# Kernel optimization log

Measured on AMD Instinct MI355X. Metric: run time of the kernel, lower is better.

Reference implementation:

```python
import jax, jax.numpy as jnp
import numpy as np
from jax import lax

EPS = 1e-5

def _per_sample_conv(x, w, stride):
    # x: [B,C,H,W], w: [B,O,I,3,3] -> one conv per sample (hypernetwork weights)
    def one(xi, wi):
        return lax.conv_general_dilated(
            xi[None], wi, window_strides=(stride, stride),
            padding=((1, 1), (1, 1)),
            dimension_numbers=('NCHW', 'OIHW', 'NCHW'))[0]
    return jax.vmap(one)(x, w)

def _batchnorm_train(x, gamma, beta):
    # torch BatchNorm2d training mode: batch stats over (N,H,W), biased var
    mean = jnp.mean(x, axis=(0, 2, 3), keepdims=True)
    var = jnp.var(x, axis=(0, 2, 3), keepdims=True)
    xn = (x - mean) * lax.rsqrt(var + EPS)
    return xn * gamma[None, :, None, None] + beta[None, :, None, None]

def setup_inputs() -> dict:
    key = jax.random.key(0)
    k1, k2, k3 = jax.random.split(key, 3)
    B, C, H, W = 32, 64, 112, 112
    x = jax.random.normal(k1, (B, C, H, W), dtype=jnp.float32)
    conv1_w = jax.random.normal(k2, (B, C, C, 3, 3), dtype=jnp.float32)
    conv2_w = jax.random.normal(k3, (B, C, C, 3, 3), dtype=jnp.float32)
    gamma1 = jnp.ones((C,), jnp.float32)
    beta1 = jnp.zeros((C,), jnp.float32)
    gamma2 = jnp.ones((C,), jnp.float32)
    beta2 = jnp.zeros((C,), jnp.float32)
    return {"x": x, "conv1_w": conv1_w, "conv2_w": conv2_w,
            "gamma1": gamma1, "beta1": beta1, "gamma2": gamma2, "beta2": beta2}

def reference(x, conv1_w, conv2_w, gamma1, beta1, gamma2, beta2):
    residual = x  # downsample=False -> IdentityLayer
    out = _per_sample_conv(x, conv1_w, stride=1)
    out = jax.nn.relu(_batchnorm_train(out, gamma1, beta1))
    out = _per_sample_conv(out, conv2_w, stride=1)
    out = _batchnorm_train(out, gamma2, beta2)
    return jax.nn.relu(out + residual)
```

## Files before the change

kernel.cpp:

```cpp
#include <hip/hip_runtime.h>

#define HW   112
#define HW2  12544
#define CH   64
#define NB   32
#define PRW  113
#define NP   12655
#define POFF 128
#define PS   13056
#define NPC  (NB*HW2)
#define TPX  784

using u16 = unsigned short;
typedef __attribute__((ext_vector_type(8))) short bf16x8;
typedef __attribute__((ext_vector_type(4))) float f32x4;

__device__ __forceinline__ float b2f(u16 u) {
    union { unsigned int i; float f; } c;
    c.i = ((unsigned int)u) << 16;
    return c.f;
}
__device__ __forceinline__ u16 f2b(float f) {
    union { float f; unsigned int i; } c;
    c.f = f;
    unsigned int x = c.i;
    x += 0x7fffu + ((x >> 16) & 1u);
    return (u16)(x >> 16);
}

template<int MODE>
__global__ __launch_bounds__(448, 2)
void conv_mfma(const u16* __restrict__ img, const u16* __restrict__ wt,
               u16* __restrict__ outp, float* __restrict__ sums,
               const float* __restrict__ psums, const float* __restrict__ gamma,
               const float* __restrict__ beta)
{
    __shared__ u16 wl[36864];
    __shared__ u16 bt[32768];
    const int bid = (int)blockIdx.x;
    const int sid = (bid & 7) * 64 + (bid >> 3);
    const int b = sid >> 4, tile = sid & 15;
    const int p0 = tile * TPX;
    const int w0 = tile * 791 - 114;
    const int tid = threadIdx.x;
    const int lane = tid & 63, wave = tid >> 6;
    const int px = lane & 15, kg = lane >> 4;

    const u16* wtb = wt + (size_t)b * 36864;
    for (int c = tid; c < 4608; c += 448)
        *(bf16x8*)(wl + c * 8) = *(const bf16x8*)(wtb + c * 8);

    float sc0[8], bi0[8], sc1[8], bi1[8];
    if (MODE == 1) {
        const int q = tid & 3;
#pragma unroll
        for (int e = 0; e < 8; ++e) {
            int c0 = q * 8 + e, c1 = 32 + q * 8 + e;
            float m0 = psums[c0] * (1.f / NPC), m1 = psums[c1] * (1.f / NPC);
            float v0 = psums[64 + c0] * (1.f / NPC) - m0 * m0;
            float v1 = psums[64 + c1] * (1.f / NPC) - m1 * m1;
            sc0[e] = gamma[c0] * rsqrtf(v0 + 1e-5f); bi0[e] = beta[c0] - m0 * sc0[e];
            sc1[e] = gamma[c1] * rsqrtf(v1 + 1e-5f); bi1[e] = beta[c1] - m1 * sc1[e];
        }
    }

    {
        const u16* bp = img + ((size_t)(b * 2 + 0) * PS + POFF + w0) * 32;
        for (int c = tid; c < 4096; c += 448) {
            bf16x8 v = *(const bf16x8*)(bp + c * 8);
            if (MODE == 1) {
                int pt = w0 + (c >> 2);
                bool val = ((unsigned)pt < (unsigned)NP) && (pt % PRW != PRW - 1);
#pragma unroll
                for (int e = 0; e < 8; ++e) {
                    float t = b2f((u16)v[e]) * sc0[e] + bi0[e];
                    t = (val && t > 0.f) ? t : 0.f;
                    v[e] = (short)f2b(t);
                }
            }
            *(bf16x8*)(bt + c * 8) = v;
        }
    }
    __syncthreads();

    int lsf[7];
#pragma unroll
    for (int f = 0; f < 7; ++f) {
        const int pix = p0 + (wave * 7 + f) * 16 + px;
        lsf[f] = pix + pix / HW - w0;
    }

    f32x4 acc[7][4];
#pragma unroll
    for (int f = 0; f < 7; ++f)
#pragma unroll
        for (int m = 0; m < 4; ++m) acc[f][m] = (f32x4)0.f;

#pragma unroll
    for (int h = 0; h < 2; ++h) {
        if (h == 1) {
            __syncthreads();
            const u16* bp = img + ((size_t)(b * 2 + 1) * PS + POFF + w0) * 32;
            for (int c = tid; c < 4096; c += 448) {
                bf16x8 v = *(const bf16x8*)(bp + c * 8);
                if (MODE == 1) {
                    int pt = w0 + (c >> 2);
                    bool val = ((unsigned)pt < (unsigned)NP) && (pt % PRW != PRW - 1);
#pragma unroll
                    for (int e = 0; e < 8; ++e) {
                        float t = b2f((u16)v[e]) * sc1[e] + bi1[e];
                        t = (val && t > 0.f) ? t : 0.f;
                        v[e] = (short)f2b(t);
                    }
                }
                *(bf16x8*)(bt + c * 8) = v;
            }
            __syncthreads();
        }
#pragma unroll
        for (int tap = 0; tap < 9; ++tap) {
            const int off = (tap / 3 - 1) * PRW + (tap % 3 - 1);
            bf16x8 Af[4];
#pragma unroll
            for (int m = 0; m < 4; ++m)
                Af[m] = *(const bf16x8*)(wl + h * 18432 + tap * 2048 + kg * 512 + (m * 16 + px) * 8);
#pragma unroll
            for (int f = 0; f < 7; ++f) {
                bf16x8 Bf = *(const bf16x8*)(bt + (lsf[f] + off) * 32 + kg * 8);
#pragma unroll
                for (int m = 0; m < 4; ++m)
                    acc[f][m] = __builtin_amdgcn_mfma_f32_16x16x32_bf16(Af[m], Bf, acc[f][m], 0, 0, 0);
            }
        }
    }

    float s_[4][4], sq[4][4];
#pragma unroll
    for (int m = 0; m < 4; ++m)
#pragma unroll
        for (int q = 0; q < 4; ++q) { s_[m][q] = 0.f; sq[m][q] = 0.f; }

#pragma unroll
    for (int f = 0; f < 7; ++f) {
        const int pix  = p0 + (wave * 7 + f) * 16 + px;
        const int slot = pix + pix / HW;
#pragma unroll
        for (int m = 0; m < 4; ++m) {
            float v0 = acc[f][m][0], v1 = acc[f][m][1], v2 = acc[f][m][2], v3 = acc[f][m][3];
            s_[m][0] += v0; s_[m][1] += v1; s_[m][2] += v2; s_[m][3] += v3;
            sq[m][0] += v0 * v0; sq[m][1] += v1 * v1;
            sq[m][2] += v2 * v2; sq[m][3] += v3 * v3;
            uint2 pk;
            pk.x = ((unsigned)f2b(v1) << 16) | f2b(v0);
            pk.y = ((unsigned)f2b(v3) << 16) | f2b(v2);
            if (MODE == 0) {
                u16* dst = outp + ((size_t)(b * 2 + (m >> 1)) * PS + POFF + slot) * 32
                                + (m & 1) * 16 + kg * 4;
                *(uint2*)dst = pk;
            } else {
                u16* dst = outp + ((size_t)b * HW2 + pix) * 64 + m * 16 + kg * 4;
                *(uint2*)dst = pk;
            }
        }
    }
#pragma unroll
    for (int off = 1; off < 16; off <<= 1) {
#pragma unroll
        for (int m = 0; m < 4; ++m)
#pragma unroll
            for (int q = 0; q < 4; ++q) {
                s_[m][q] += __shfl_xor(s_[m][q], off);
                sq[m][q] += __shfl_xor(sq[m][q], off);
            }
    }
    __syncthreads();
    float* red = (float*)bt;
    if (px == 0) {
#pragma unroll
        for (int m = 0; m < 4; ++m)
#pragma unroll
            for (int q = 0; q < 4; ++q) {
                int c = m * 16 + kg * 4 + q;
                red[wave * 128 + c]      = s_[m][q];
                red[wave * 128 + 64 + c] = sq[m][q];
            }
    }
    __syncthreads();
    if (tid < 128) {
        float t = 0.f;
#pragma unroll
        for (int k = 0; k < 7; ++k) t += red[k * 128 + tid];
        atomicAdd(&sums[tid], t);
    }
}

__global__ __launch_bounds__(256)
void xpad_kernel(const float* __restrict__ x, u16* __restrict__ img)
{
    const int b  = blockIdx.y;
    const int y  = blockIdx.x * 2 + (threadIdx.x >> 7);
    const int px = threadIdx.x & 127;
    if (px >= HW) return;
    const float* xr = x + (size_t)b * CH * HW2 + (size_t)y * HW + px;
#pragma unroll
    for (int cg = 0; cg < 8; ++cg) {
        bf16x8 pk;
#pragma unroll
        for (int j = 0; j < 8; ++j)
            pk[j] = (short)f2b(xr[(size_t)(cg * 8 + j) * HW2]);
        u16* op = img + ((size_t)(b * 2 + (cg >> 2)) * PS + POFF + (size_t)y * PRW + px) * 32
                      + (cg & 3) * 8;
        *(bf16x8*)op = pk;
    }
}

__global__ void border_kernel(u16* __restrict__ a, u16* __restrict__ y1,
                              float* __restrict__ st)
{
    if (blockIdx.x == 256) {
        if (threadIdx.x < 256) st[threadIdx.x] = 0.f;
        return;
    }
    int t = blockIdx.x * 256 + threadIdx.x;
    u16* buf = (t >= 32768) ? y1 : a;
    int t2 = t & 32767;
    int bh = t2 >> 9;
    int s  = t2 & 511;
    int slot;
    if (s < POFF)            slot = s;
    else if (s < POFF + 273) slot = POFF + NP + (s - POFF);
    else                     slot = POFF + (s - (POFF + 273)) * PRW + (PRW - 1);
    float4* q = (float4*)(buf + ((size_t)bh * PS + slot) * 32);
#pragma unroll
    for (int i = 0; i < 4; ++i) q[i] = (float4){0.f, 0.f, 0.f, 0.f};
}

__global__ __launch_bounds__(256)
void repack2_kernel(const float* __restrict__ w1, const float* __restrict__ w2,
                    u16* __restrict__ wt1, u16* __restrict__ wt2)
{
    int i = blockIdx.x * 256 + threadIdx.x;
    const int N = NB * 36864;
    const float* w = (i < N) ? w1 : w2;
    u16* wt = (i < N) ? wt1 : wt2;
    int o = (i < N) ? i : i - N;
    int b = o / 36864, r = o - b * 36864;
    int half = r / 18432; r -= half * 18432;
    int tap  = r / 2048;  r -= tap * 2048;
    int kq   = r / 512;   r -= kq * 512;
    int co   = r / 8;
    int ci   = half * 32 + kq * 8 + (r & 7);
    wt[o] = f2b(w[(((size_t)b * 64 + co) * 64 + ci) * 9 + tap]);
}

__global__ __launch_bounds__(256)
void finalize_kernel(const u16* __restrict__ y2, const float* __restrict__ sums,
                     const float* __restrict__ gamma, const float* __restrict__ beta,
                     const float* __restrict__ x, float* __restrict__ out)
{
    __shared__ float lt[64][116];
    __shared__ float sbl[128];
    const int b = blockIdx.y, y = blockIdx.x;
    const int tid = threadIdx.x;
    if (tid < 64) {
        float mean = sums[tid] * (1.f / NPC);
        float var  = sums[64 + tid] * (1.f / NPC) - mean * mean;
        float sc   = gamma[tid] * rsqrtf(var + 1e-5f);
        sbl[tid]      = sc;
        sbl[64 + tid] = beta[tid] - mean * sc;
    }
    __syncthreads();
    const u16* rowp = y2 + ((size_t)b * HW2 + (size_t)y * HW) * 64;
    {
        const int cg = tid & 7;
        float sc[8], bi[8];
#pragma unroll
        for (int e = 0; e < 8; ++e) { sc[e] = sbl[cg * 8 + e]; bi[e] = sbl[64 + cg * 8 + e]; }
        for (int t = tid; t < HW * 8; t += 256) {
            int px = t >> 3;
            bf16x8 v = *(const bf16x8*)(rowp + px * 64 + cg * 8);
#pragma unroll
            for (int e = 0; e < 8; ++e)
                lt[cg * 8 + e][px] = b2f((u16)v[e]) * sc[e] + bi[e];
        }
    }
    __syncthreads();
    {
        const int c = tid >> 2, xg = (tid & 3) * 28;
        size_t base = ((size_t)b * CH + c) * HW2 + (size_t)y * HW + xg;
#pragma unroll
        for (int i = 0; i < 7; ++i) {
            float4 xv = *(const float4*)(x + base + i * 4);
            float4 r;
            r.x = fmaxf(lt[c][xg + i * 4 + 0] + xv.x, 0.f);
            r.y = fmaxf(lt[c][xg + i * 4 + 1] + xv.y, 0.f);
            r.z = fmaxf(lt[c][xg + i * 4 + 2] + xv.z, 0.f);
            r.w = fmaxf(lt[c][xg + i * 4 + 3] + xv.w, 0.f);
            *(float4*)(out + base + i * 4) = r;
        }
    }
}

extern "C" void kernel_launch(void* const* d_in, const int* in_sizes, int n_in,
                              void* d_out, int out_size, void* d_ws, size_t ws_size,
                              hipStream_t stream)
{
    const float* x  = (const float*)d_in[0];
    const float* w1 = (const float*)d_in[1];
    const float* w2 = (const float*)d_in[2];
    const float* g1 = (const float*)d_in[3];
    const float* b1 = (const float*)d_in[4];
    const float* g2 = (const float*)d_in[5];
    const float* b2 = (const float*)d_in[6];
    float* out = (float*)d_out;

    char* ws = (char*)d_ws;
    u16*   imgA = (u16*)ws;
    u16*   y2c  = (u16*)ws;
    float* st   = (float*)(ws + (size_t)(56u << 20));
    float* sums1 = st, *sums2 = st + 128;
    char*  oc   = (char*)d_out;
    u16*   y1p  = (u16*)oc;
    u16*   wt1  = (u16*)(oc + (size_t)(54u << 20));
    u16*   wt2  = (u16*)(oc + (size_t)(58u << 20));

    border_kernel<<<257, 256, 0, stream>>>(imgA, y1p, st);
    xpad_kernel<<<dim3(56, 32), 256, 0, stream>>>(x, imgA);
    repack2_kernel<<<9216, 256, 0, stream>>>(w1, w2, wt1, wt2);

    conv_mfma<0><<<512, 448, 0, stream>>>(imgA, wt1, y1p, sums1, st, g1, b1);
    conv_mfma<1><<<512, 448, 0, stream>>>(y1p, wt2, y2c, sums2, sums1, g1, b1);
    finalize_kernel<<<dim3(112, 32), 256, 0, stream>>>(y2c, sums2, g2, b2, x, out);
}
```

Baseline: 217.7 us.

## Shrink conv tiles to 256 pixels and prefetch second channel half into registers

Each conv block now covers 256 pixels with 4 waves instead of 784 pixels with 7 waves, giving 1568 blocks instead of 512. Shared memory holds only half of the weights and half of the input channels at a time. The second half's weights and activations are loaded into registers before the first MMA pass, so the global loads overlap compute, then written to shared memory between the two passes. This aims at better load balance across CUs and at hiding load latency, at the cost of more halo reloading, more per-block weight loads and higher register pressure from the prefetch buffers.

Result: no change. 222.1 us (+2.0%).

```diff
diff --git a/kernel.cpp b/kernel.cpp
--- a/kernel.cpp
+++ b/kernel.cpp
@@ -9,7 +9,7 @@
 #define POFF 128
 #define PS   13056
 #define NPC  (NB*HW2)
-#define TPX  784
+#define TPX  256
 
 using u16 = unsigned short;
 typedef __attribute__((ext_vector_type(8))) short bf16x8;
@@ -28,27 +28,46 @@
     return (u16)(x >> 16);
 }
 
+__device__ __forceinline__ void kloop(const u16* __restrict__ wl,
+                                      const u16* __restrict__ bt,
+                                      const int* lsf, int kg, int px,
+                                      f32x4 (&acc)[4][4])
+{
+#pragma unroll
+    for (int tap = 0; tap < 9; ++tap) {
+        const int off = (tap / 3 - 1) * PRW + (tap % 3 - 1);
+        bf16x8 Af[4];
+#pragma unroll
+        for (int m = 0; m < 4; ++m)
+            Af[m] = *(const bf16x8*)(wl + tap * 2048 + kg * 512 + (m * 16 + px) * 8);
+#pragma unroll
+        for (int f = 0; f < 4; ++f) {
+            bf16x8 Bf = *(const bf16x8*)(bt + (lsf[f] + off) * 32 + kg * 8);
+#pragma unroll
+            for (int m = 0; m < 4; ++m)
+                acc[f][m] = __builtin_amdgcn_mfma_f32_16x16x32_bf16(Af[m], Bf, acc[f][m], 0, 0, 0);
+        }
+    }
+}
+
 template<int MODE>
-__global__ __launch_bounds__(448, 2)
+__global__ __launch_bounds__(256, 2)
 void conv_mfma(const u16* __restrict__ img, const u16* __restrict__ wt,
                u16* __restrict__ outp, float* __restrict__ sums,
                const float* __restrict__ psums, const float* __restrict__ gamma,
                const float* __restrict__ beta)
 {
-    __shared__ u16 wl[36864];
-    __shared__ u16 bt[32768];
+    __shared__ u16 wl[18432];
+    __shared__ u16 bt[16384];
     const int bid = (int)blockIdx.x;
-    const int sid = (bid & 7) * 64 + (bid >> 3);
-    const int b = sid >> 4, tile = sid & 15;
+    const int sid = (bid & 7) * 196 + (bid >> 3);
+    const int b = sid / 49, tile = sid - b * 49;
     const int p0 = tile * TPX;
-    const int w0 = tile * 791 - 114;
+    const int w0 = p0 + p0 / HW - 114;
     const int tid = threadIdx.x;
     const int lane = tid & 63, wave = tid >> 6;
     const int px = lane & 15, kg = lane >> 4;
-
     const u16* wtb = wt + (size_t)b * 36864;
-    for (int c = tid; c < 4608; c += 448)
-        *(bf16x8*)(wl + c * 8) = *(const bf16x8*)(wtb + c * 8);
 
     float sc0[8], bi0[8], sc1[8], bi1[8];
     if (MODE == 1) {
@@ -65,8 +84,15 @@
     }
 
     {
+#pragma unroll
+        for (int i = 0; i < 9; ++i) {
+            const int c = tid + i * 256;
+            *(bf16x8*)(wl + c * 8) = *(const bf16x8*)(wtb + c * 8);
+        }
         const u16* bp = img + ((size_t)(b * 2 + 0) * PS + POFF + w0) * 32;
-        for (int c = tid; c < 4096; c += 448) {
+#pragma unroll
+        for (int i = 0; i < 8; ++i) {
+            const int c = tid + i * 256;
             bf16x8 v = *(const bf16x8*)(bp + c * 8);
             if (MODE == 1) {
                 int pt = w0 + (c >> 2);
@@ -83,56 +109,56 @@
     }
     __syncthreads();
 
-    int lsf[7];
-#pragma unroll
-    for (int f = 0; f < 7; ++f) {
-        const int pix = p0 + (wave * 7 + f) * 16 + px;
+    bf16x8 wpre[9], bpre[8];
+#pragma unroll
+    for (int i = 0; i < 9; ++i)
+        wpre[i] = *(const bf16x8*)(wtb + 18432 + (tid + i * 256) * 8);
+    {
+        const u16* bp = img + ((size_t)(b * 2 + 1) * PS + POFF + w0) * 32;
+#pragma unroll
+        for (int i = 0; i < 8; ++i)
+            bpre[i] = *(const bf16x8*)(bp + (tid + i * 256) * 8);
+    }
+    __builtin_amdgcn_sched_barrier(0);
+
+    int lsf[4];
+#pragma unroll
+    for (int f = 0; f < 4; ++f) {
+        const int pix = p0 + wave * 64 + f * 16 + px;
         lsf[f] = pix + pix / HW - w0;
     }
 
-    f32x4 acc[7][4];
-#pragma unroll
-    for (int f = 0; f < 7; ++f)
+    f32x4 acc[4][4];
+#pragma unroll
+    for (int f = 0; f < 4; ++f)
 #pragma unroll
         for (int m = 0; m < 4; ++m) acc[f][m] = (f32x4)0.f;
 
-#pragma unroll
-    for (int h = 0; h < 2; ++h) {
-        if (h == 1) {
-            __syncthreads();
-            const u16* bp = img + ((size_t)(b * 2 + 1) * PS + POFF + w0) * 32;
-            for (int c = tid; c < 4096; c += 448) {
-                bf16x8 v = *(const bf16x8*)(bp + c * 8);
-                if (MODE == 1) {
-                    int pt = w0 + (c >> 2);
-                    bool val = ((unsigned)pt < (unsigned)NP) && (pt % PRW != PRW - 1);
-#pragma unroll
-                    for (int e = 0; e < 8; ++e) {
-                        float t = b2f((u16)v[e]) * sc1[e] + bi1[e];
-                        t = (val && t > 0.f) ? t : 0.f;
-                        v[e] = (short)f2b(t);
-                    }
-                }
-                *(bf16x8*)(bt + c * 8) = v;
-            }
-            __syncthreads();
-        }
-#pragma unroll
-        for (int tap = 0; tap < 9; ++tap) {
-            const int off = (tap / 3 - 1) * PRW + (tap % 3 - 1);
-            bf16x8 Af[4];
-#pragma unroll
-            for (int m = 0; m < 4; ++m)
-                Af[m] = *(const bf16x8*)(wl + h * 18432 + tap * 2048 + kg * 512 + (m * 16 + px) * 8);
-#pragma unroll
-            for (int f = 0; f < 7; ++f) {
-                bf16x8 Bf = *(const bf16x8*)(bt + (lsf[f] + off) * 32 + kg * 8);
-#pragma unroll
-                for (int m = 0; m < 4; ++m)
-                    acc[f][m] = __builtin_amdgcn_mfma_f32_16x16x32_bf16(Af[m], Bf, acc[f][m], 0, 0, 0);
-            }
-        }
-    }
+    kloop(wl, bt, lsf, kg, px, acc);
+    __syncthreads();
+
+#pragma unroll
+    for (int i = 0; i < 9; ++i)
+        *(bf16x8*)(wl + (tid + i * 256) * 8) = wpre[i];
+#pragma unroll
+    for (int i = 0; i < 8; ++i) {
+        bf16x8 v = bpre[i];
+        if (MODE == 1) {
+            const int c = tid + i * 256;
+            int pt = w0 + (c >> 2);
+            bool val = ((unsigned)pt < (unsigned)NP) && (pt % PRW != PRW - 1);
+#pragma unroll
+            for (int e = 0; e < 8; ++e) {
+                float t = b2f((u16)v[e]) * sc1[e] + bi1[e];
+                t = (val && t > 0.f) ? t : 0.f;
+                v[e] = (short)f2b(t);
+            }
+        }
+        *(bf16x8*)(bt + (tid + i * 256) * 8) = v;
+    }
+    __syncthreads();
+
+    kloop(wl, bt, lsf, kg, px, acc);
 
     float s_[4][4], sq[4][4];
 #pragma unroll
@@ -141,8 +167,8 @@
         for (int q = 0; q < 4; ++q) { s_[m][q] = 0.f; sq[m][q] = 0.f; }
 
 #pragma unroll
-    for (int f = 0; f < 7; ++f) {
-        const int pix  = p0 + (wave * 7 + f) * 16 + px;
+    for (int f = 0; f < 4; ++f) {
+        const int pix  = p0 + wave * 64 + f * 16 + px;
         const int slot = pix + pix / HW;
 #pragma unroll
         for (int m = 0; m < 4; ++m) {
@@ -187,9 +213,7 @@
     }
     __syncthreads();
     if (tid < 128) {
-        float t = 0.f;
-#pragma unroll
-        for (int k = 0; k < 7; ++k) t += red[k * 128 + tid];
+        float t = red[tid] + red[128 + tid] + red[256 + tid] + red[384 + tid];
         atomicAdd(&sums[tid], t);
     }
 }
@@ -328,7 +352,7 @@
     xpad_kernel<<<dim3(56, 32), 256, 0, stream>>>(x, imgA);
     repack2_kernel<<<9216, 256, 0, stream>>>(w1, w2, wt1, wt2);
 
-    conv_mfma<0><<<512, 448, 0, stream>>>(imgA, wt1, y1p, sums1, st, g1, b1);
-    conv_mfma<1><<<512, 448, 0, stream>>>(y1p, wt2, y2c, sums2, sums1, g1, b1);
+    conv_mfma<0><<<1568, 256, 0, stream>>>(imgA, wt1, y1p, sums1, st, g1, b1);
+    conv_mfma<1><<<1568, 256, 0, stream>>>(y1p, wt2, y2c, sums2, sums1, g1, b1);
     finalize_kernel<<<dim3(112, 32), 256, 0, stream>>>(y2c, sums2, g2, b2, x, out);
 }
```
